# Kernel tuning notes

Measured on AMD Instinct MI355X. Metric: run time of the kernel, lower is better.

Reference implementation:

```python
import jax, jax.numpy as jnp
import numpy as np
import math

# Config: 8 packed images, each a 32x32 patch grid (t=1) -> equal seglen 1024
NSEG, GH, GW = 8, 32, 32
L = GH * GW            # 1024 tokens per segment
S = NSEG * L           # 8192 packed tokens
H, NH = 1024, 16
HD = H // NH           # 64, head dim (rope dim), divisible by 4
MLP = 4096
THETA = 10000.0


def _make_rope_cos_sin():
    # Rope2DPosEmb._precompute_freqs_cis for a (GH, GW) grid, dim=HD
    flat = np.arange(L, dtype=np.float32)
    x_pos = flat % GW
    y_pos = flat // GW
    dim_range = np.arange(0, HD, 4, dtype=np.float32)[: HD // 4]
    freqs = 1.0 / THETA ** (dim_range / HD)          # [HD//4]
    x_f = np.outer(x_pos, freqs)                     # [L, HD//4]
    y_f = np.outer(y_pos, freqs)
    # interleave x/y angles per frequency -> [L, HD//2]
    ang = np.stack([x_f, y_f], axis=-1).reshape(L, HD // 2)
    ang = np.tile(ang, (NSEG, 1))                    # same grid repeated per image
    return jnp.asarray(np.cos(ang)), jnp.asarray(np.sin(ang))


def setup_inputs() -> dict:
    key = jax.random.key(0)
    ks = jax.random.split(key, 8)
    cos, sin = _make_rope_cos_sin()
    inp = {
        "x": jax.random.normal(ks[0], (S, H), jnp.float32),
        "wqkv": jax.random.normal(ks[1], (3 * H, H), jnp.float32) * math.sqrt(1.0 / H),
        "wo": jax.random.normal(ks[2], (H, H), jnp.float32) * math.sqrt(1.0 / H),
        "ln0_g": jnp.ones((H,), jnp.float32),
        "ln0_b": jnp.zeros((H,), jnp.float32),
        "ln1_g": jnp.ones((H,), jnp.float32),
        "ln1_b": jnp.zeros((H,), jnp.float32),
        "fc0_w": jax.random.normal(ks[3], (MLP, H), jnp.float32) * math.sqrt(2.0 / H),
        "fc0_b": jnp.zeros((MLP,), jnp.float32),
        "fc1_w": jax.random.normal(ks[4], (H, MLP), jnp.float32) * math.sqrt(2.0 / MLP),
        "fc1_b": jnp.zeros((H,), jnp.float32),
        "rope_cos": cos,
        "rope_sin": sin,
        "cu_seqlens": jnp.arange(NSEG + 1, dtype=jnp.int32) * L,
    }
    return inp


def _layernorm(x, g, b, eps=1e-5):
    m = x.mean(-1, keepdims=True)
    v = ((x - m) ** 2).mean(-1, keepdims=True)
    return (x - m) * jax.lax.rsqrt(v + eps) * g + b


def _apply_rope(x, cos, sin):
    # x: [S, NH, HD]; cos/sin: [S, HD//2]. Complex mult on (even, odd) pairs.
    xr = x.reshape(S, NH, HD // 2, 2)
    x0, x1 = xr[..., 0], xr[..., 1]
    c = cos[:, None, :]
    s = sin[:, None, :]
    o0 = x0 * c - x1 * s
    o1 = x0 * s + x1 * c
    return jnp.stack([o0, o1], axis=-1).reshape(S, NH, HD)


def reference(x, wqkv, wo, ln0_g, ln0_b, ln1_g, ln1_b,
              fc0_w, fc0_b, fc1_w, fc1_b, rope_cos, rope_sin, cu_seqlens):
    # --- attention branch (pre-norm) ---
    h = _layernorm(x, ln0_g, ln0_b)
    qkv = (h @ wqkv.T).reshape(S, 3, NH, HD)
    q, k, v = qkv[:, 0], qkv[:, 1], qkv[:, 2]
    q = _apply_rope(q, rope_cos, rope_sin)
    k = _apply_rope(k, rope_cos, rope_sin)
    # block-diagonal varlen attention: equal-length segments -> reshape
    qb = q.reshape(NSEG, L, NH, HD)
    kb = k.reshape(NSEG, L, NH, HD)
    vb = v.reshape(NSEG, L, NH, HD)
    scores = jnp.einsum("blhd,bmhd->bhlm", qb, kb) / math.sqrt(HD)
    p = jax.nn.softmax(scores.astype(jnp.float32), axis=-1).astype(x.dtype)
    attn = jnp.einsum("bhlm,bmhd->blhd", p, vb).reshape(S, H)
    x = x + attn @ wo.T
    # --- MLP branch (pre-norm) ---
    h2 = _layernorm(x, ln1_g, ln1_b)
    mlp = jax.nn.gelu(h2 @ fc0_w.T + fc0_b, approximate=False) @ fc1_w.T + fc1_b
    return x + mlp
```

## Files before the change

### kernel.cpp

```cpp
#include <hip/hip_runtime.h>
#include <math.h>


typedef __bf16 bf16x8 __attribute__((ext_vector_type(8)));
typedef float f32x4 __attribute__((ext_vector_type(4)));

__device__ __forceinline__ unsigned short f2b(float f) {
  unsigned u = __float_as_uint(f);
  return (unsigned short)((u + 0x7FFFu + ((u >> 16) & 1u)) >> 16);
}
__device__ __forceinline__ float b2f(unsigned short h) {
  return __uint_as_float(((unsigned)h) << 16);
}
__device__ __forceinline__ void async_ld16(const void* g, void* l) {
  __builtin_amdgcn_global_load_lds((__attribute__((address_space(1))) void*)g,
                                   (__attribute__((address_space(3))) void*)l,
                                   16, 0, 0);
}
__device__ __forceinline__ float exp2fast(float x) {
#if __has_builtin(__builtin_amdgcn_exp2f)
  return __builtin_amdgcn_exp2f(x);
#else
  return exp2f(x);
#endif
}

__global__ __launch_bounds__(256) void castw_kernel(const float* __restrict__ src,
                                                    unsigned short* __restrict__ dst,
                                                    int n4) {
  int t = blockIdx.x * 256 + threadIdx.x;
  if (t >= n4) return;
  float4 v = ((const float4*)src)[t];
  ushort4 o;
  o.x = f2b(v.x); o.y = f2b(v.y); o.z = f2b(v.z); o.w = f2b(v.w);
  ((ushort4*)dst)[t] = o;
}

__global__ __launch_bounds__(256) void ln_kernel(const float* __restrict__ x,
                                                 const float* __restrict__ g,
                                                 const float* __restrict__ bt,
                                                 unsigned short* __restrict__ out) {
  __shared__ float red[8];
  const int row = blockIdx.x, t = threadIdx.x;
  const float4 v = ((const float4*)(x + (size_t)row * 1024))[t];
  float s = v.x + v.y + v.z + v.w;
  float s2 = v.x * v.x + v.y * v.y + v.z * v.z + v.w * v.w;
#pragma unroll
  for (int m = 1; m < 64; m <<= 1) {
    s += __shfl_xor(s, m, 64);
    s2 += __shfl_xor(s2, m, 64);
  }
  if ((t & 63) == 0) { red[t >> 6] = s; red[4 + (t >> 6)] = s2; }
  __syncthreads();
  const float ts = red[0] + red[1] + red[2] + red[3];
  const float ts2 = red[4] + red[5] + red[6] + red[7];
  const float mean = ts * (1.f / 1024.f);
  const float var = ts2 * (1.f / 1024.f) - mean * mean;
  const float inv = rsqrtf(var + 1e-5f);
  const float4 gv = ((const float4*)g)[t];
  const float4 bv = ((const float4*)bt)[t];
  ushort4 o;
  o.x = f2b((v.x - mean) * inv * gv.x + bv.x);
  o.y = f2b((v.y - mean) * inv * gv.y + bv.y);
  o.z = f2b((v.z - mean) * inv * gv.z + bv.z);
  o.w = f2b((v.w - mean) * inv * gv.w + bv.w);
  ((ushort4*)out)[(size_t)row * 256 + t] = o;
}

template <int MODE>
__global__ __launch_bounds__(256) void gemm_bt(
    const unsigned short* __restrict__ A, const unsigned short* __restrict__ B,
    int M, int N, int K, float* __restrict__ outf, unsigned short* __restrict__ outb,
    const float* __restrict__ res, const float* __restrict__ bias) {
  __shared__ __align__(16) unsigned short As[128 * 32];
  __shared__ __align__(16) unsigned short Bs[128 * 32];
  const int bm = blockIdx.y * 128, bn = blockIdx.x * 128;
  const int t = threadIdx.x, wave = t >> 6, lane = t & 63;
  const int quad = lane >> 4, l16 = lane & 15;
  const int wm = (wave >> 1) * 64, wn = (wave & 1) * 64;
  const int srow = lane >> 2;
  const int scol = (((lane & 3) ^ ((lane >> 3) & 3)) * 8);
  const unsigned short* Ag0 = A + (size_t)(bm + wave * 32 + srow) * K + scol;
  const unsigned short* Ag1 = Ag0 + (size_t)16 * K;
  const unsigned short* Bg0 = B + (size_t)(bn + wave * 32 + srow) * K + scol;
  const unsigned short* Bg1 = Bg0 + (size_t)16 * K;
  unsigned short* Al = As + wave * 1024;
  unsigned short* Bl = Bs + wave * 1024;
  const int swg = (l16 >> 1) & 3;
  f32x4 acc[4][4] = {};
  for (int k0 = 0; k0 < K; k0 += 32) {
    async_ld16(Ag0 + k0, Al);
    async_ld16(Ag1 + k0, Al + 512);
    async_ld16(Bg0 + k0, Bl);
    async_ld16(Bg1 + k0, Bl + 512);
    __syncthreads();
    bf16x8 af[4], bfv[4];
#pragma unroll
    for (int i = 0; i < 4; i++)
      af[i] = *(const bf16x8*)(As + (wm + i * 16 + l16) * 32 + (quad ^ swg) * 8);
#pragma unroll
    for (int j = 0; j < 4; j++)
      bfv[j] = *(const bf16x8*)(Bs + (wn + j * 16 + l16) * 32 + (quad ^ swg) * 8);
#pragma unroll
    for (int i = 0; i < 4; i++)
#pragma unroll
      for (int j = 0; j < 4; j++)
        acc[i][j] = __builtin_amdgcn_mfma_f32_16x16x32_bf16(af[i], bfv[j], acc[i][j], 0, 0, 0);
    __syncthreads();
  }
#pragma unroll
  for (int i = 0; i < 4; i++)
#pragma unroll
    for (int j = 0; j < 4; j++)
#pragma unroll
      for (int r = 0; r < 4; r++) {
        const int m = bm + wm + i * 16 + quad * 4 + r;
        const int n = bn + wn + j * 16 + l16;
        const size_t idx = (size_t)m * N + n;
        const float v = acc[i][j][r];
        if (MODE == 1) {
          outf[idx] = v + res[idx];
        } else if (MODE == 2) {
          const float z = v + bias[n];
          outb[idx] = f2b(0.5f * z * (1.f + erff(z * 0.70710678f)));
        } else if (MODE == 3) {
          outf[idx] = v + bias[n] + res[idx];
        } else {
          outb[idx] = f2b(v);
        }
      }
}

__global__ __launch_bounds__(256) void rope_kernel(const unsigned short* __restrict__ qkv,
                                                   const float* __restrict__ cb,
                                                   const float* __restrict__ sb,
                                                   unsigned short* __restrict__ qh,
                                                   unsigned short* __restrict__ kh) {
  const int tid = blockIdx.x * 256 + threadIdx.x;
  const int i = tid & 31, head = (tid >> 5) & 15, s = tid >> 9;
  const float c = cb[s * 32 + i], sn = sb[s * 32 + i];
  const unsigned short* base = qkv + (size_t)s * 3072 + head * 64 + 2 * i;
  const float q0 = b2f(base[0]), q1 = b2f(base[1]);
  const float k0 = b2f(base[1024]), k1 = b2f(base[1025]);
  const int seg = s >> 10, l = s & 1023;
  const size_t o = ((size_t)((seg * 16 + head) * 1024 + l)) * 64 + 2 * i;
  const float QSC = 0.125f * 1.44269504f;
  ushort2 qo, ko;
  qo.x = f2b((q0 * c - q1 * sn) * QSC);
  qo.y = f2b((q0 * sn + q1 * c) * QSC);
  ko.x = f2b(k0 * c - k1 * sn);
  ko.y = f2b(k0 * sn + k1 * c);
  *(ushort2*)(qh + o) = qo;
  *(ushort2*)(kh + o) = ko;
}

__global__ __launch_bounds__(256) void vtrans_kernel(const unsigned short* __restrict__ qkv,
                                                     unsigned short* __restrict__ vt) {
  __shared__ unsigned short tile[64][72];
  const int b = blockIdx.x;
  const int lt = b & 15, head = (b >> 4) & 15, seg = b >> 8;
  const int t = threadIdx.x;
  const int r = t >> 2, c0 = (t & 3) * 16;
  const unsigned short* src =
      qkv + ((size_t)(seg * 1024 + lt * 64 + r)) * 3072 + 2048 + head * 64 + c0;
#pragma unroll
  for (int k = 0; k < 16; k++) tile[r][c0 + k] = src[k];
  __syncthreads();
  unsigned short* dst =
      vt + ((size_t)((seg * 16 + head) * 64 + r)) * 1024 + lt * 64 + c0;
#pragma unroll
  for (int k = 0; k < 16; k++) dst[k] = tile[c0 + k][r];
}

__global__ __launch_bounds__(256) void attn_kernel(const unsigned short* __restrict__ qh,
                                                   const unsigned short* __restrict__ kh,
                                                   const unsigned short* __restrict__ vt,
                                                   unsigned short* __restrict__ out) {
  __shared__ __align__(16) unsigned short Qs[128 * 64];
  __shared__ __align__(16) unsigned short Ks[64 * 64];
  __shared__ __align__(16) unsigned short Vs[64 * 64];
  __shared__ __align__(16) __bf16 Ps[128 * 68];
  const int b = blockIdx.x;
  const int head = b & 15, seg = (b >> 4) & 7, qt = b >> 7;
  const int t = threadIdx.x, wave = t >> 6, lane = t & 63;
  const int quad = lane >> 4, l16 = lane & 15;
  const size_t sh = (size_t)(seg * 16 + head);
  const unsigned short* qbase = qh + (sh * 1024 + (size_t)qt * 128) * 64;
  const unsigned short* kbase = kh + sh * 1024 * 64;
  const unsigned short* vbase = vt + sh * 64 * 1024;
  const int r8 = lane >> 3;
  const int c8 = ((lane & 7) ^ (r8 & 7)) * 8;
#pragma unroll
  for (int cc = 0; cc < 4; cc++) {
    const int chunk = wave * 4 + cc;
    async_ld16(qbase + (size_t)(chunk * 8 + r8) * 64 + c8, Qs + chunk * 512);
  }
  float lsum[2][4] = {};
  f32x4 o_acc[2][4] = {};
  const int sw = l16 & 7;

  for (int kt = 0; kt < 16; kt++) {
    const int ch0 = wave * 2;
    async_ld16(kbase + (size_t)(kt * 64 + ch0 * 8 + r8) * 64 + c8, Ks + ch0 * 512);
    async_ld16(kbase + (size_t)(kt * 64 + ch0 * 8 + 8 + r8) * 64 + c8, Ks + ch0 * 512 + 512);
    async_ld16(vbase + (size_t)(ch0 * 8 + r8) * 1024 + kt * 64 + c8, Vs + ch0 * 512);
    async_ld16(vbase + (size_t)(ch0 * 8 + 8 + r8) * 1024 + kt * 64 + c8, Vs + ch0 * 512 + 512);
    __syncthreads();
    f32x4 s[2][4] = {};
#pragma unroll
    for (int ks = 0; ks < 2; ks++) {
      const int co = ((ks * 4 + quad) ^ sw) * 8;
      bf16x8 aq[2], bk[4];
#pragma unroll
      for (int i = 0; i < 2; i++)
        aq[i] = *(const bf16x8*)(Qs + (wave * 32 + i * 16 + l16) * 64 + co);
#pragma unroll
      for (int j = 0; j < 4; j++)
        bk[j] = *(const bf16x8*)(Ks + (j * 16 + l16) * 64 + co);
#pragma unroll
      for (int i = 0; i < 2; i++)
#pragma unroll
        for (int j = 0; j < 4; j++)
          s[i][j] = __builtin_amdgcn_mfma_f32_16x16x32_bf16(aq[i], bk[j], s[i][j], 0, 0, 0);
    }
#pragma unroll
    for (int i = 0; i < 2; i++)
#pragma unroll
      for (int r = 0; r < 4; r++) {
        const float p0 = exp2fast(s[i][0][r]);
        const float p1 = exp2fast(s[i][1][r]);
        const float p2 = exp2fast(s[i][2][r]);
        const float p3 = exp2fast(s[i][3][r]);
        lsum[i][r] += (p0 + p1) + (p2 + p3);
        const int prow = wave * 32 + i * 16 + quad * 4 + r;
        __bf16* pb = Ps + prow * 68 + l16;
        pb[0]  = (__bf16)p0;
        pb[16] = (__bf16)p1;
        pb[32] = (__bf16)p2;
        pb[48] = (__bf16)p3;
      }
#pragma unroll
    for (int ks = 0; ks < 2; ks++) {
      const int co = ((ks * 4 + quad) ^ sw) * 8;
      bf16x8 bv[4];
#pragma unroll
      for (int j = 0; j < 4; j++)
        bv[j] = *(const bf16x8*)(Vs + (j * 16 + l16) * 64 + co);
#pragma unroll
      for (int i = 0; i < 2; i++) {
        const bf16x8 ap = *(const bf16x8*)(Ps + (wave * 32 + i * 16 + l16) * 68 + ks * 32 + quad * 8);
#pragma unroll
        for (int j = 0; j < 4; j++)
          o_acc[i][j] = __builtin_amdgcn_mfma_f32_16x16x32_bf16(ap, bv[j], o_acc[i][j], 0, 0, 0);
      }
    }
    __syncthreads();
  }
#pragma unroll
  for (int i = 0; i < 2; i++)
#pragma unroll
    for (int r = 0; r < 4; r++) {
      float l = lsum[i][r];
      l += __shfl_xor(l, 1, 64);
      l += __shfl_xor(l, 2, 64);
      l += __shfl_xor(l, 4, 64);
      l += __shfl_xor(l, 8, 64);
      const float invl = 1.0f / l;
      const int qrow = seg * 1024 + qt * 128 + wave * 32 + i * 16 + quad * 4 + r;
#pragma unroll
      for (int j = 0; j < 4; j++)
        out[(size_t)qrow * 1024 + head * 64 + j * 16 + l16] = f2b(o_acc[i][j][r] * invl);
    }
}

extern "C" void kernel_launch(void* const* d_in, const int* in_sizes, int n_in,
                              void* d_out, int out_size, void* d_ws, size_t ws_size,
                              hipStream_t stream) {
  (void)in_sizes; (void)n_in; (void)out_size; (void)ws_size;
  const float* x    = (const float*)d_in[0];
  const float* wqkv = (const float*)d_in[1];
  const float* wo   = (const float*)d_in[2];
  const float* ln0g = (const float*)d_in[3];
  const float* ln0b = (const float*)d_in[4];
  const float* ln1g = (const float*)d_in[5];
  const float* ln1b = (const float*)d_in[6];
  const float* fc0w = (const float*)d_in[7];
  const float* fc0b = (const float*)d_in[8];
  const float* fc1w = (const float*)d_in[9];
  const float* fc1b = (const float*)d_in[10];
  const float* rc   = (const float*)d_in[11];
  const float* rsn  = (const float*)d_in[12];
  float* out = (float*)d_out;
  char* w = (char*)d_ws;
  const size_t MB = 1u << 20;
  unsigned short* hb    = (unsigned short*)(w + 0);
  unsigned short* bqkv  = (unsigned short*)(w + 16 * MB);
  unsigned short* bwo   = (unsigned short*)(w + 22 * MB);
  unsigned short* bfc0  = (unsigned short*)(w + 24 * MB);
  unsigned short* bfc1  = (unsigned short*)(w + 32 * MB);
  unsigned short* qhb   = (unsigned short*)(w + 40 * MB);
  unsigned short* khb   = (unsigned short*)(w + 56 * MB);
  unsigned short* vtb   = (unsigned short*)(w + 72 * MB);
  unsigned short* attnb = (unsigned short*)(w + 88 * MB);
  unsigned short* qkvb  = (unsigned short*)(w + 104 * MB);
  unsigned short* midb  = (unsigned short*)(w + 104 * MB);

  castw_kernel<<<3072, 256, 0, stream>>>(wqkv, bqkv, 786432);
  castw_kernel<<<1024, 256, 0, stream>>>(wo, bwo, 262144);
  castw_kernel<<<4096, 256, 0, stream>>>(fc0w, bfc0, 1048576);
  castw_kernel<<<4096, 256, 0, stream>>>(fc1w, bfc1, 1048576);
  ln_kernel<<<8192, 256, 0, stream>>>(x, ln0g, ln0b, hb);
  gemm_bt<4><<<dim3(24, 64), 256, 0, stream>>>(hb, bqkv, 8192, 3072, 1024,
                                               nullptr, qkvb, nullptr, nullptr);
  rope_kernel<<<16384, 256, 0, stream>>>(qkvb, rc, rsn, qhb, khb);
  vtrans_kernel<<<2048, 256, 0, stream>>>(qkvb, vtb);
  attn_kernel<<<1024, 256, 0, stream>>>(qhb, khb, vtb, attnb);
  gemm_bt<1><<<dim3(8, 64), 256, 0, stream>>>(attnb, bwo, 8192, 1024, 1024,
                                              out, nullptr, x, nullptr);
  ln_kernel<<<8192, 256, 0, stream>>>(out, ln1g, ln1b, hb);
  gemm_bt<2><<<dim3(32, 64), 256, 0, stream>>>(hb, bfc0, 8192, 4096, 1024,
                                               nullptr, midb, nullptr, fc0b);
  gemm_bt<3><<<dim3(8, 64), 256, 0, stream>>>(midb, bfc1, 8192, 1024, 4096,
                                              out, nullptr, out, fc1b);
}
```

Baseline: 562.9 us.

## Rework attention to 32x32 MFMA with register-resident P, vectorize rope, fuse casts

The attention kernel moves from 16x16x32 to 32x32x16 MFMAs. It computes S^T so the softmax probabilities stay in registers and are exchanged across half-waves with shuffles, instead of round-tripping through an LDS P buffer. The row-sum is reduced via a small LDS array. Rope now processes 8 elements per thread with 128-bit loads and stores. The four weight-cast launches are merged into one kernel. The erf GELU in the fc0 epilogue is replaced by a tanh-form approximation built from exp2 and a fast reciprocal, which slightly changes numerics against the exact-GELU reference.

```diff
diff --git a/kernel.cpp b/kernel.cpp
--- a/kernel.cpp
+++ b/kernel.cpp
@@ -4,6 +4,8 @@
 
 typedef __bf16 bf16x8 __attribute__((ext_vector_type(8)));
 typedef float f32x4 __attribute__((ext_vector_type(4)));
+typedef float f32x16 __attribute__((ext_vector_type(16)));
+typedef unsigned int u32;
 
 __device__ __forceinline__ unsigned short f2b(float f) {
   unsigned u = __float_as_uint(f);
@@ -24,13 +26,26 @@
   return exp2f(x);
 #endif
 }
-
-__global__ __launch_bounds__(256) void castw_kernel(const float* __restrict__ src,
-                                                    unsigned short* __restrict__ dst,
-                                                    int n4) {
-  int t = blockIdx.x * 256 + threadIdx.x;
-  if (t >= n4) return;
-  float4 v = ((const float4*)src)[t];
+__device__ __forceinline__ float rcpfast(float x) {
+#if __has_builtin(__builtin_amdgcn_rcpf)
+  return __builtin_amdgcn_rcpf(x);
+#else
+  return 1.0f / x;
+#endif
+}
+
+__global__ __launch_bounds__(256) void castall_kernel(
+    const float* __restrict__ s0, const float* __restrict__ s1,
+    const float* __restrict__ s2, const float* __restrict__ s3,
+    unsigned short* __restrict__ dst) {
+  const int t = blockIdx.x * 256 + threadIdx.x;
+  const float* src;
+  int off;
+  if (t < 786432) { src = s0; off = t; }
+  else if (t < 1048576) { src = s1; off = t - 786432; }
+  else if (t < 2097152) { src = s2; off = t - 1048576; }
+  else { src = s3; off = t - 2097152; }
+  const float4 v = ((const float4*)src)[off];
   ushort4 o;
   o.x = f2b(v.x); o.y = f2b(v.y); o.z = f2b(v.z); o.w = f2b(v.w);
   ((ushort4*)dst)[t] = o;
@@ -122,7 +137,10 @@
           outf[idx] = v + res[idx];
         } else if (MODE == 2) {
           const float z = v + bias[n];
-          outb[idx] = f2b(0.5f * z * (1.f + erff(z * 0.70710678f)));
+          const float u = z * (0.7978845608f + 0.03567740814f * z * z);
+          const float e = fminf(u * 2.885390082f, 80.f);
+          const float tt = exp2fast(e);
+          outb[idx] = f2b(z * tt * rcpfast(tt + 1.0f));
         } else if (MODE == 3) {
           outf[idx] = v + bias[n] + res[idx];
         } else {
@@ -131,27 +149,33 @@
       }
 }
 
+__device__ __forceinline__ u32 rope2(u32 in, float c, float sn, float sc) {
+  const float a = b2f((unsigned short)(in & 0xffff));
+  const float b = b2f((unsigned short)(in >> 16));
+  return (u32)f2b((a * c - b * sn) * sc) | ((u32)f2b((a * sn + b * c) * sc) << 16);
+}
 __global__ __launch_bounds__(256) void rope_kernel(const unsigned short* __restrict__ qkv,
                                                    const float* __restrict__ cb,
                                                    const float* __restrict__ sb,
                                                    unsigned short* __restrict__ qh,
                                                    unsigned short* __restrict__ kh) {
   const int tid = blockIdx.x * 256 + threadIdx.x;
-  const int i = tid & 31, head = (tid >> 5) & 15, s = tid >> 9;
-  const float c = cb[s * 32 + i], sn = sb[s * 32 + i];
-  const unsigned short* base = qkv + (size_t)s * 3072 + head * 64 + 2 * i;
-  const float q0 = b2f(base[0]), q1 = b2f(base[1]);
-  const float k0 = b2f(base[1024]), k1 = b2f(base[1025]);
+  const int ii = tid & 7, head = (tid >> 3) & 15, s = tid >> 7;
+  const float4 cv = *(const float4*)(cb + s * 32 + ii * 4);
+  const float4 sv = *(const float4*)(sb + s * 32 + ii * 4);
+  const unsigned short* base = qkv + (size_t)s * 3072 + head * 64 + ii * 8;
+  const uint4 qa = *(const uint4*)base;
+  const uint4 ka = *(const uint4*)(base + 1024);
   const int seg = s >> 10, l = s & 1023;
-  const size_t o = ((size_t)((seg * 16 + head) * 1024 + l)) * 64 + 2 * i;
+  const size_t o = ((size_t)((seg * 16 + head) * 1024 + l)) * 64 + ii * 8;
   const float QSC = 0.125f * 1.44269504f;
-  ushort2 qo, ko;
-  qo.x = f2b((q0 * c - q1 * sn) * QSC);
-  qo.y = f2b((q0 * sn + q1 * c) * QSC);
-  ko.x = f2b(k0 * c - k1 * sn);
-  ko.y = f2b(k0 * sn + k1 * c);
-  *(ushort2*)(qh + o) = qo;
-  *(ushort2*)(kh + o) = ko;
+  uint4 qo, ko;
+  qo.x = rope2(qa.x, cv.x, sv.x, QSC); ko.x = rope2(ka.x, cv.x, sv.x, 1.f);
+  qo.y = rope2(qa.y, cv.y, sv.y, QSC); ko.y = rope2(ka.y, cv.y, sv.y, 1.f);
+  qo.z = rope2(qa.z, cv.z, sv.z, QSC); ko.z = rope2(ka.z, cv.z, sv.z, 1.f);
+  qo.w = rope2(qa.w, cv.w, sv.w, QSC); ko.w = rope2(ka.w, cv.w, sv.w, 1.f);
+  *(uint4*)(qh + o) = qo;
+  *(uint4*)(kh + o) = ko;
 }
 
 __global__ __launch_bounds__(256) void vtrans_kernel(const unsigned short* __restrict__ qkv,
@@ -179,11 +203,11 @@
   __shared__ __align__(16) unsigned short Qs[128 * 64];
   __shared__ __align__(16) unsigned short Ks[64 * 64];
   __shared__ __align__(16) unsigned short Vs[64 * 64];
-  __shared__ __align__(16) __bf16 Ps[128 * 68];
+  __shared__ float wl[128];
   const int b = blockIdx.x;
   const int head = b & 15, seg = (b >> 4) & 7, qt = b >> 7;
   const int t = threadIdx.x, wave = t >> 6, lane = t & 63;
-  const int quad = lane >> 4, l16 = lane & 15;
+  const int h = lane >> 5, q31 = lane & 31;
   const size_t sh = (size_t)(seg * 16 + head);
   const unsigned short* qbase = qh + (sh * 1024 + (size_t)qt * 128) * 64;
   const unsigned short* kbase = kh + sh * 1024 * 64;
@@ -195,9 +219,11 @@
     const int chunk = wave * 4 + cc;
     async_ld16(qbase + (size_t)(chunk * 8 + r8) * 64 + c8, Qs + chunk * 512);
   }
-  float lsum[2][4] = {};
-  f32x4 o_acc[2][4] = {};
-  const int sw = l16 & 7;
+  const int qrow_l = wave * 32 + q31;
+  const int qsw = qrow_l & 7;
+  bf16x8 qf[4];
+  float lsum = 0.f;
+  f32x16 oacc[2] = {};
 
   for (int kt = 0; kt < 16; kt++) {
     const int ch0 = wave * 2;
@@ -206,71 +232,87 @@
     async_ld16(vbase + (size_t)(ch0 * 8 + r8) * 1024 + kt * 64 + c8, Vs + ch0 * 512);
     async_ld16(vbase + (size_t)(ch0 * 8 + 8 + r8) * 1024 + kt * 64 + c8, Vs + ch0 * 512 + 512);
     __syncthreads();
-    f32x4 s[2][4] = {};
-#pragma unroll
-    for (int ks = 0; ks < 2; ks++) {
-      const int co = ((ks * 4 + quad) ^ sw) * 8;
-      bf16x8 aq[2], bk[4];
-#pragma unroll
-      for (int i = 0; i < 2; i++)
-        aq[i] = *(const bf16x8*)(Qs + (wave * 32 + i * 16 + l16) * 64 + co);
-#pragma unroll
-      for (int j = 0; j < 4; j++)
-        bk[j] = *(const bf16x8*)(Ks + (j * 16 + l16) * 64 + co);
-#pragma unroll
-      for (int i = 0; i < 2; i++)
-#pragma unroll
-        for (int j = 0; j < 4; j++)
-          s[i][j] = __builtin_amdgcn_mfma_f32_16x16x32_bf16(aq[i], bk[j], s[i][j], 0, 0, 0);
-    }
-#pragma unroll
-    for (int i = 0; i < 2; i++)
-#pragma unroll
-      for (int r = 0; r < 4; r++) {
-        const float p0 = exp2fast(s[i][0][r]);
-        const float p1 = exp2fast(s[i][1][r]);
-        const float p2 = exp2fast(s[i][2][r]);
-        const float p3 = exp2fast(s[i][3][r]);
-        lsum[i][r] += (p0 + p1) + (p2 + p3);
-        const int prow = wave * 32 + i * 16 + quad * 4 + r;
-        __bf16* pb = Ps + prow * 68 + l16;
-        pb[0]  = (__bf16)p0;
-        pb[16] = (__bf16)p1;
-        pb[32] = (__bf16)p2;
-        pb[48] = (__bf16)p3;
+    if (kt == 0) {
+#pragma unroll
+      for (int ks = 0; ks < 4; ks++)
+        qf[ks] = *(const bf16x8*)(Qs + qrow_l * 64 + (((2 * ks + h) ^ qsw)) * 8);
+    }
+    f32x16 st[2] = {{}, {}};
+#pragma unroll
+    for (int T = 0; T < 2; T++) {
+      const int krow = 32 * T + q31;
+      const int ksw = krow & 7;
+#pragma unroll
+      for (int ks = 0; ks < 4; ks++) {
+        const bf16x8 kf = *(const bf16x8*)(Ks + krow * 64 + (((2 * ks + h) ^ ksw)) * 8);
+        st[T] = __builtin_amdgcn_mfma_f32_32x32x16_bf16(kf, qf[ks], st[T], 0, 0, 0);
       }
-#pragma unroll
-    for (int ks = 0; ks < 2; ks++) {
-      const int co = ((ks * 4 + quad) ^ sw) * 8;
-      bf16x8 bv[4];
-#pragma unroll
-      for (int j = 0; j < 4; j++)
-        bv[j] = *(const bf16x8*)(Vs + (j * 16 + l16) * 64 + co);
-#pragma unroll
-      for (int i = 0; i < 2; i++) {
-        const bf16x8 ap = *(const bf16x8*)(Ps + (wave * 32 + i * 16 + l16) * 68 + ks * 32 + quad * 8);
-#pragma unroll
-        for (int j = 0; j < 4; j++)
-          o_acc[i][j] = __builtin_amdgcn_mfma_f32_16x16x32_bf16(ap, bv[j], o_acc[i][j], 0, 0, 0);
+    }
+    u32 pk[2][4][2];
+#pragma unroll
+    for (int T = 0; T < 2; T++)
+#pragma unroll
+      for (int g = 0; g < 4; g++)
+#pragma unroll
+        for (int e = 0; e < 2; e++) {
+          const float plo = exp2fast(st[T][4 * g + 2 * e]);
+          const float phi = exp2fast(st[T][4 * g + 2 * e + 1]);
+          lsum += plo + phi;
+          pk[T][g][e] = (u32)f2b(plo) | ((u32)f2b(phi) << 16);
+        }
+    u32 rcv[2][4];
+#pragma unroll
+    for (int T = 0; T < 2; T++) {
+      const u32 p0 = h ? pk[T][0][0] : pk[T][1][0];
+      const u32 p1 = h ? pk[T][0][1] : pk[T][1][1];
+      const u32 p2 = h ? pk[T][2][0] : pk[T][3][0];
+      const u32 p3 = h ? pk[T][2][1] : pk[T][3][1];
+      rcv[T][0] = (u32)__shfl_xor((int)p0, 32, 64);
+      rcv[T][1] = (u32)__shfl_xor((int)p1, 32, 64);
+      rcv[T][2] = (u32)__shfl_xor((int)p2, 32, 64);
+      rcv[T][3] = (u32)__shfl_xor((int)p3, 32, 64);
+    }
+#pragma unroll
+    for (int tt = 0; tt < 4; tt++) {
+      const int T = tt >> 1, uu = tt & 1;
+      union { u32 u[4]; bf16x8 v; } af;
+      if (h == 0) {
+        af.u[0] = pk[T][2 * uu][0];
+        af.u[1] = pk[T][2 * uu][1];
+        af.u[2] = rcv[T][2 * uu];
+        af.u[3] = rcv[T][2 * uu + 1];
+      } else {
+        af.u[0] = rcv[T][2 * uu];
+        af.u[1] = rcv[T][2 * uu + 1];
+        af.u[2] = pk[T][2 * uu + 1][0];
+        af.u[3] = pk[T][2 * uu + 1][1];
       }
+#pragma unroll
+      for (int ot = 0; ot < 2; ot++) {
+        const int vrow = 32 * ot + q31;
+        const int vsw = vrow & 7;
+        const bf16x8 bv = *(const bf16x8*)(Vs + vrow * 64 + (((2 * tt + h) ^ vsw)) * 8);
+        oacc[ot] = __builtin_amdgcn_mfma_f32_32x32x16_bf16(af.v, bv, oacc[ot], 0, 0, 0);
+      }
     }
     __syncthreads();
   }
-#pragma unroll
-  for (int i = 0; i < 2; i++)
-#pragma unroll
-    for (int r = 0; r < 4; r++) {
-      float l = lsum[i][r];
-      l += __shfl_xor(l, 1, 64);
-      l += __shfl_xor(l, 2, 64);
-      l += __shfl_xor(l, 4, 64);
-      l += __shfl_xor(l, 8, 64);
-      const float invl = 1.0f / l;
-      const int qrow = seg * 1024 + qt * 128 + wave * 32 + i * 16 + quad * 4 + r;
-#pragma unroll
-      for (int j = 0; j < 4; j++)
-        out[(size_t)qrow * 1024 + head * 64 + j * 16 + l16] = f2b(o_acc[i][j][r] * invl);
-    }
+  lsum += __shfl_xor(lsum, 32, 64);
+  if (h == 0) wl[wave * 32 + q31] = lsum;
+  const int qglob = seg * 1024 + qt * 128 + wave * 32;
+#pragma unroll
+  for (int g = 0; g < 4; g++) {
+    const float4 lv = *(const float4*)&wl[wave * 32 + 8 * g + 4 * h];
+#pragma unroll
+    for (int m = 0; m < 4; m++) {
+      const int r16 = 4 * g + m;
+      const int qrow = qglob + m + 8 * g + 4 * h;
+      const float invl = rcpfast((&lv.x)[m]);
+#pragma unroll
+      for (int ot = 0; ot < 2; ot++)
+        out[(size_t)qrow * 1024 + head * 64 + 32 * ot + q31] = f2b(oacc[ot][r16] * invl);
+    }
+  }
 }
 
 extern "C" void kernel_launch(void* const* d_in, const int* in_sizes, int n_in,
@@ -305,14 +347,11 @@
   unsigned short* qkvb  = (unsigned short*)(w + 104 * MB);
   unsigned short* midb  = (unsigned short*)(w + 104 * MB);
 
-  castw_kernel<<<3072, 256, 0, stream>>>(wqkv, bqkv, 786432);
-  castw_kernel<<<1024, 256, 0, stream>>>(wo, bwo, 262144);
-  castw_kernel<<<4096, 256, 0, stream>>>(fc0w, bfc0, 1048576);
-  castw_kernel<<<4096, 256, 0, stream>>>(fc1w, bfc1, 1048576);
+  castall_kernel<<<12288, 256, 0, stream>>>(wqkv, wo, fc0w, fc1w, bqkv);
   ln_kernel<<<8192, 256, 0, stream>>>(x, ln0g, ln0b, hb);
   gemm_bt<4><<<dim3(24, 64), 256, 0, stream>>>(hb, bqkv, 8192, 3072, 1024,
                                                nullptr, qkvb, nullptr, nullptr);
-  rope_kernel<<<16384, 256, 0, stream>>>(qkvb, rc, rsn, qhb, khb);
+  rope_kernel<<<4096, 256, 0, stream>>>(qkvb, rc, rsn, qhb, khb);
   vtrans_kernel<<<2048, 256, 0, stream>>>(qkvb, vtb);
   attn_kernel<<<1024, 256, 0, stream>>>(qhb, khb, vtb, attnb);
   gemm_bt<1><<<dim3(8, 64), 256, 0, stream>>>(attnb, bwo, 8192, 1024, 1024,
```

After: 545.7 us. 3.1% less time.
